# Optimization experiments

Measured on AMD Instinct MI355X. Metric: run time of the kernel, lower is better.

Reference implementation:

```python
import jax, jax.numpy as jnp
import numpy as np

N = 50000   # nodes
E = 800000  # edges
D = 64      # hidden_channels (= in_channels)
L = 3       # num_layers
G = 512     # graphs in batch
S = 32      # s_channels
BN_EPS = 1e-5


def setup_inputs() -> dict:
    key = jax.random.key(0)
    ks = jax.random.split(key, 10)
    x = jax.random.normal(ks[0], (N, D), dtype=jnp.float32)
    edge_index = jax.random.randint(ks[1], (2, E), 0, N)
    batch = jnp.sort(jax.random.randint(ks[2], (N,), 0, G))
    mapping = jax.random.randint(ks[3], (G,), 0, N)
    edge_weight = jax.random.uniform(ks[4], (E,), dtype=jnp.float32)
    pooling_mask = jnp.ones((N,), dtype=jnp.float32)
    # per-layer GIN MLP params (stacked over layers)
    W1 = 0.05 * jax.random.normal(ks[5], (L, D, D), dtype=jnp.float32)
    b1 = jnp.zeros((L, D), jnp.float32)
    gamma = jnp.ones((L, D), jnp.float32)
    beta = jnp.zeros((L, D), jnp.float32)
    bn_mean = jnp.zeros((L, D), jnp.float32)
    bn_var = jnp.ones((L, D), jnp.float32)
    W2 = 0.05 * jax.random.normal(ks[6], (L, D, D), dtype=jnp.float32)
    b2 = jnp.zeros((L, D), jnp.float32)
    eps = jnp.zeros((L,), jnp.float32)  # train_eps=True, init 0
    lin_w = 0.05 * jax.random.normal(ks[7], (2 * D * L, S), dtype=jnp.float32)
    lin_b = jnp.zeros((S,), jnp.float32)
    return dict(x=x, edge_weight=edge_weight, pooling_mask=pooling_mask,
                W1=W1, b1=b1, gamma=gamma, beta=beta, bn_mean=bn_mean,
                bn_var=bn_var, W2=W2, b2=b2, eps=eps, lin_w=lin_w,
                lin_b=lin_b, edge_index=edge_index, batch=batch,
                mapping=mapping)


def _sgin_forward(x, edge_weight, pooling_mask, W1, b1, gamma, beta,
                  bn_mean, bn_var, W2, b2, eps, lin_w, lin_b,
                  edge_index, batch, mapping):
    src, dst = edge_index[0], edge_index[1]
    h = x  # dropout is identity in eval mode
    pooled = []
    for i in range(L):
        # GIN aggregation: sum_j w_ij * h_j  at target nodes
        msg = h[src] * edge_weight[:, None]            # [E, D]
        agg = jax.ops.segment_sum(msg, dst, num_segments=N)
        z = (1.0 + eps[i]) * h + agg                   # [N, D]
        # MLP: Linear -> BN(eval) -> ReLU -> Linear -> ReLU
        z = z @ W1[i] + b1[i]
        z = gamma[i] * (z - bn_mean[i]) * jax.lax.rsqrt(bn_var[i] + BN_EPS) + beta[i]
        z = jax.nn.relu(z)
        h = jax.nn.relu(z @ W2[i] + b2[i])
        # per-layer pooling: masked global add pool || center-node gather
        emb_add = jax.ops.segment_sum(h * pooling_mask[:, None], batch,
                                      num_segments=G)  # [G, D]
        emb_center = h[mapping]                          # [G, D]
        pooled.append(jnp.concatenate([emb_add, emb_center], axis=-1))
    hcat = jnp.concatenate(pooled, axis=1)               # [G, 2*D*L]
    return hcat @ lin_w + lin_b                          # [G, S]


def reference(x, edge_weight, pooling_mask, W1, b1, gamma, beta, bn_mean,
              bn_var, W2, b2, eps, lin_w, lin_b, edge_index, batch, mapping):
    return _sgin_forward(x, edge_weight, pooling_mask, W1, b1, gamma, beta,
                         bn_mean, bn_var, W2, b2, eps, lin_w, lin_b,
                         edge_index, batch, mapping)
```

## Files before the change

kernel.cpp:

```cpp
#include <hip/hip_runtime.h>
#include <hip/hip_fp16.h>

#define DD 64
#define HC 384
#define SS 32
#define BINW 256
#define BSH 8
#define CAP 8192
#define CHUNK 2048

typedef _Float16 f16x8v __attribute__((ext_vector_type(8)));
typedef float f32x4v __attribute__((ext_vector_type(4)));

__global__ __launch_bounds__(256) void prep_kernel(
    const float* __restrict__ x, __half* __restrict__ hh0,
    int* __restrict__ bin_cur, float* __restrict__ hcat,
    const float* __restrict__ W1, const float* __restrict__ W2,
    const float* __restrict__ gma, const float* __restrict__ bta,
    const float* __restrict__ bnm, const float* __restrict__ bnv,
    const float* __restrict__ b1, __half* __restrict__ wpk,
    float* __restrict__ abbn, int nbins, int hcat4, int total)
{
  int gid = blockIdx.x * 256 + threadIdx.x;
  if (gid < nbins) bin_cur[gid] = gid * CAP;
  if (gid < hcat4) ((float4*)hcat)[gid] = make_float4(0.f, 0.f, 0.f, 0.f);
  if (gid < 3072) {
    int lane_ = gid & 63;
    int rest = gid >> 6;
    int kb = rest & 1;
    int nt = (rest >> 1) & 3;
    int gm = (rest >> 3) & 1;
    int ly = rest >> 4;
    const float* W = gm ? W2 : W1;
    int c = nt * 16 + (lane_ & 15);
    int k0 = kb * 32 + (lane_ >> 4) * 8;
    f16x8v o;
    #pragma unroll
    for (int j = 0; j < 8; ++j)
      o[j] = (_Float16)W[((size_t)ly * DD + k0 + j) * DD + c];
    *(f16x8v*)(wpk + gid * 8) = o;
  }
  if (gid >= 4096 && gid < 4288) {
    int id = gid - 4096;
    int ly = id >> 6, c = id & 63;
    float A = gma[ly * DD + c] * rsqrtf(bnv[ly * DD + c] + 1e-5f);
    float B = fmaf(b1[ly * DD + c] - bnm[ly * DD + c], A, bta[ly * DD + c]);
    abbn[ly * 128 + c] = A;
    abbn[ly * 128 + 64 + c] = B;
  }
  int i = gid * 8;
  if (i < total) {
    float4 a = *(const float4*)(x + i);
    float4 b = *(const float4*)(x + i + 4);
    __half2 o[4];
    o[0] = __floats2half2_rn(a.x, a.y);
    o[1] = __floats2half2_rn(a.z, a.w);
    o[2] = __floats2half2_rn(b.x, b.y);
    o[3] = __floats2half2_rn(b.z, b.w);
    *(float4*)(hh0 + i) = *(float4*)o;
  }
}

__global__ __launch_bounds__(256) void bin_part_kernel(
    const int* __restrict__ ei, const float* __restrict__ ew,
    int* __restrict__ bin_cur, unsigned* __restrict__ pk_slab,
    unsigned short* __restrict__ dl_slab, int E)
{
  __shared__ unsigned spk[CHUNK];
  __shared__ unsigned short sdst[CHUNK];
  __shared__ int bcnt[256], boff[256], bcur[256], gbase[256], stmp[256];
  int t = threadIdx.x;
  int e0 = blockIdx.x * CHUNK;
  int m = min(CHUNK, E - e0);
  bcnt[t] = 0;
  __syncthreads();
  for (int i = t; i < m; i += 256)
    atomicAdd(&bcnt[ei[E + e0 + i] >> BSH], 1);
  __syncthreads();
  int v = bcnt[t];
  stmp[t] = v;
  __syncthreads();
  for (int o = 1; o < 256; o <<= 1) {
    int u = (t >= o) ? stmp[t - o] : 0;
    __syncthreads();
    stmp[t] += u;
    __syncthreads();
  }
  boff[t] = stmp[t] - v;
  bcur[t] = stmp[t] - v;
  if (v > 0) gbase[t] = atomicAdd(&bin_cur[t], v);
  __syncthreads();
  for (int i = t; i < m; i += 256) {
    unsigned d = (unsigned)ei[E + e0 + i];
    int b = d >> BSH;
    int p = atomicAdd(&bcur[b], 1);
    unsigned short wh = __half_as_ushort(__float2half(ew[e0 + i]));
    spk[p] = (unsigned)ei[e0 + i] | ((unsigned)wh << 16);
    sdst[p] = (unsigned short)d;
  }
  __syncthreads();
  for (int i = t; i < m; i += 256) {
    unsigned short d = sdst[i];
    int b = d >> BSH;
    int g = gbase[b] + (i - boff[b]);
    pk_slab[g] = spk[i];
    dl_slab[g] = d;
  }
}

__global__ __launch_bounds__(256) void fine_csr_kernel(
    const unsigned* __restrict__ pk_slab,
    const unsigned short* __restrict__ dl_slab,
    const int* __restrict__ bin_cur, int* __restrict__ beg,
    int* __restrict__ endo, unsigned* __restrict__ packed, int N)
{
  __shared__ int cnt[256], loff[256], cur[256], stmp[256];
  int t = threadIdx.x;
  int b = blockIdx.x;
  int sbase = b * CAP;
  int m = bin_cur[b] - sbase;
  cnt[t] = 0;
  __syncthreads();
  for (int i = t; i < m; i += 256)
    atomicAdd(&cnt[dl_slab[sbase + i] & 255], 1);
  __syncthreads();
  int v = cnt[t];
  stmp[t] = v;
  __syncthreads();
  for (int o = 1; o < 256; o <<= 1) {
    int u = (t >= o) ? stmp[t - o] : 0;
    __syncthreads();
    stmp[t] += u;
    __syncthreads();
  }
  loff[t] = stmp[t] - v;
  cur[t] = loff[t];
  int node = b * BINW + t;
  if (node < N) {
    beg[node] = sbase + loff[t];
    endo[node] = sbase + loff[t] + v;
  }
  __syncthreads();
  for (int i = t; i < m; i += 256) {
    int dl = dl_slab[sbase + i] & 255;
    int p = atomicAdd(&cur[dl], 1);
    packed[sbase + p] = pk_slab[sbase + i];
  }
}

__global__ __launch_bounds__(256) void gather_kernel(
    const __half* __restrict__ hh, const unsigned* __restrict__ packed,
    const int* __restrict__ begA, const int* __restrict__ endA,
    const float* __restrict__ epsv, __half* __restrict__ zh, int layer, int N)
{
  int wave = threadIdx.x >> 6;
  int lane = threadIdx.x & 63;
  int sub = lane >> 3;
  int ch0 = (lane & 7) * 8;
  int na = blockIdx.x * 8 + wave * 2;
  int nb = na + 1;
  if (na >= N) return;
  bool hasB = nb < N;
  int bega = begA[na], enda = endA[na];
  int begb = hasB ? begA[nb] : 0, endb = hasB ? endA[nb] : 0;
  float accA[8] = {0, 0, 0, 0, 0, 0, 0, 0};
  float accB[8] = {0, 0, 0, 0, 0, 0, 0, 0};
  int ea = bega + sub, eb = begb + sub;
  while (ea < enda || eb < endb) {
    bool va = ea < enda;
    bool vb = eb < endb;
    unsigned pa = 0, pb = 0;
    if (va) pa = packed[ea];
    if (vb) pb = packed[eb];
    float4 ra, rb;
    if (va) ra = *(const float4*)(hh + (size_t)(pa & 0xffffu) * DD + ch0);
    if (vb) rb = *(const float4*)(hh + (size_t)(pb & 0xffffu) * DD + ch0);
    if (va) {
      float w = __half2float(__ushort_as_half((unsigned short)(pa >> 16)));
      const __half2* H = (const __half2*)&ra;
      #pragma unroll
      for (int j = 0; j < 4; ++j) {
        float2 f = __half22float2(H[j]);
        accA[2 * j]     = fmaf(w, f.x, accA[2 * j]);
        accA[2 * j + 1] = fmaf(w, f.y, accA[2 * j + 1]);
      }
    }
    if (vb) {
      float w = __half2float(__ushort_as_half((unsigned short)(pb >> 16)));
      const __half2* H = (const __half2*)&rb;
      #pragma unroll
      for (int j = 0; j < 4; ++j) {
        float2 f = __half22float2(H[j]);
        accB[2 * j]     = fmaf(w, f.x, accB[2 * j]);
        accB[2 * j + 1] = fmaf(w, f.y, accB[2 * j + 1]);
      }
    }
    ea += 8; eb += 8;
  }
  #pragma unroll
  for (int j = 0; j < 8; ++j) {
    accA[j] += __shfl_xor(accA[j], 8);
    accA[j] += __shfl_xor(accA[j], 16);
    accA[j] += __shfl_xor(accA[j], 32);
    accB[j] += __shfl_xor(accB[j], 8);
    accB[j] += __shfl_xor(accB[j], 16);
    accB[j] += __shfl_xor(accB[j], 32);
  }
  if (sub == 0) {
    float e1 = 1.0f + epsv[layer];
    {
      float4 sr = *(const float4*)(hh + (size_t)na * DD + ch0);
      const __half2* S = (const __half2*)&sr;
      f16x8v q;
      #pragma unroll
      for (int j = 0; j < 4; ++j) {
        float2 f = __half22float2(S[j]);
        q[2 * j]     = (_Float16)fmaf(e1, f.x, accA[2 * j]);
        q[2 * j + 1] = (_Float16)fmaf(e1, f.y, accA[2 * j + 1]);
      }
      *(f16x8v*)(zh + (size_t)na * DD + ch0) = q;
    }
    if (hasB) {
      float4 sr = *(const float4*)(hh + (size_t)nb * DD + ch0);
      const __half2* S = (const __half2*)&sr;
      f16x8v q;
      #pragma unroll
      for (int j = 0; j < 4; ++j) {
        float2 f = __half22float2(S[j]);
        q[2 * j]     = (_Float16)fmaf(e1, f.x, accB[2 * j]);
        q[2 * j + 1] = (_Float16)fmaf(e1, f.y, accB[2 * j + 1]);
      }
      *(f16x8v*)(zh + (size_t)nb * DD + ch0) = q;
    }
  }
}

__global__ __launch_bounds__(256) void node_mfma_kernel(
    const __half* __restrict__ zh, __half* __restrict__ hhout,
    const __half* __restrict__ wpk, const float* __restrict__ abbn,
    const float* __restrict__ b2, const float* __restrict__ pmask,
    const int* __restrict__ batch, float* __restrict__ hcat,
    int layer, int N)
{
  __shared__ float tileF[DD * DD];
  __half* tileH = (__half*)tileF;
  const int wave = threadIdx.x >> 6;
  const int lane = threadIdx.x & 63;
  const int g = lane >> 4;
  const int cr = lane & 15;
  const int n0 = blockIdx.x * 64;
  const int mrow = n0 + wave * 16 + cr;

  const __half* wl  = wpk + (size_t)layer * 8192;
  const __half* w2l = wl + 4096;

  f16x8v a0 = *(const f16x8v*)(zh + (size_t)mrow * DD + g * 8);
  f16x8v a1 = *(const f16x8v*)(zh + (size_t)mrow * DD + 32 + g * 8);
  f32x4v acc[4];
  #pragma unroll
  for (int nt = 0; nt < 4; ++nt) {
    f16x8v b0 = *(const f16x8v*)(wl + (nt * 2 + 0) * 512 + lane * 8);
    f16x8v b1 = *(const f16x8v*)(wl + (nt * 2 + 1) * 512 + lane * 8);
    acc[nt] = (f32x4v){0.f, 0.f, 0.f, 0.f};
    acc[nt] = __builtin_amdgcn_mfma_f32_16x16x32_f16(a0, b0, acc[nt], 0, 0, 0);
    acc[nt] = __builtin_amdgcn_mfma_f32_16x16x32_f16(a1, b1, acc[nt], 0, 0, 0);
  }
  #pragma unroll
  for (int nt = 0; nt < 4; ++nt) {
    int c = nt * 16 + cr;
    float Ab = abbn[layer * 128 + c];
    float Bb = abbn[layer * 128 + 64 + c];
    #pragma unroll
    for (int r = 0; r < 4; ++r) {
      int row = wave * 16 + g * 4 + r;
      float v = fmaxf(fmaf(acc[nt][r], Ab, Bb), 0.f);
      tileH[row * DD + (((c >> 3) ^ (row & 7)) * 8) + (c & 7)] = __float2half(v);
    }
  }
  __syncthreads();
  const int arow = wave * 16 + cr;
  f16x8v a20 = *(const f16x8v*)(tileH + arow * DD + ((g ^ (arow & 7)) * 8));
  f16x8v a21 = *(const f16x8v*)(tileH + arow * DD + (((4 + g) ^ (arow & 7)) * 8));
  f32x4v acc2[4];
  #pragma unroll
  for (int nt = 0; nt < 4; ++nt) {
    f16x8v b0 = *(const f16x8v*)(w2l + (nt * 2 + 0) * 512 + lane * 8);
    f16x8v b1 = *(const f16x8v*)(w2l + (nt * 2 + 1) * 512 + lane * 8);
    acc2[nt] = (f32x4v){0.f, 0.f, 0.f, 0.f};
    acc2[nt] = __builtin_amdgcn_mfma_f32_16x16x32_f16(a20, b0, acc2[nt], 0, 0, 0);
    acc2[nt] = __builtin_amdgcn_mfma_f32_16x16x32_f16(a21, b1, acc2[nt], 0, 0, 0);
  }
  __syncthreads();
  #pragma unroll
  for (int nt = 0; nt < 4; ++nt) {
    int c = nt * 16 + cr;
    float bb = b2[layer * DD + c];
    #pragma unroll
    for (int r = 0; r < 4; ++r) {
      int row = wave * 16 + g * 4 + r;
      tileF[row * DD + ((c + row) & 63)] = fmaxf(acc2[nt][r] + bb, 0.f);
    }
  }
  __syncthreads();
  #pragma unroll
  for (int i = 0; i < 2; ++i) {
    int id = i * 256 + threadIdx.x;
    int rw = id >> 3, q = id & 7;
    if (n0 + rw < N) {
      f16x8v hv;
      #pragma unroll
      for (int j = 0; j < 8; ++j)
        hv[j] = (_Float16)tileF[rw * DD + ((q * 8 + j + rw) & 63)];
      *(f16x8v*)(hhout + (size_t)(n0 + rw) * DD + q * 8) = hv;
    }
  }
  float accp = 0.0f;
  int gcur = -1;
  for (int i = 0; i < 16; ++i) {
    int r = wave * 16 + i;
    int n = n0 + r;
    if (n >= N) break;
    float v = tileF[r * DD + ((lane + r) & 63)];
    int gb = batch[n];
    if (gb != gcur) {
      if (gcur >= 0) atomicAdd(&hcat[gcur * HC + layer * 128 + lane], accp);
      gcur = gb; accp = 0.0f;
    }
    accp = fmaf(v, pmask[n], accp);
  }
  if (gcur >= 0) atomicAdd(&hcat[gcur * HC + layer * 128 + lane], accp);
}

__global__ __launch_bounds__(256) void final_kernel(
    const float* __restrict__ hcat, const __half* __restrict__ h1,
    const __half* __restrict__ h2, const __half* __restrict__ h3,
    const int* __restrict__ mapping, const float* __restrict__ lw,
    const float* __restrict__ lb, float* __restrict__ out, int G)
{
  int gid = blockIdx.x * 256 + threadIdx.x;
  int g = gid >> 5, s = gid & 31;
  if (g >= G) return;
  float acc = lb[s];
  size_t mrow = (size_t)mapping[g] * DD;
  #pragma unroll
  for (int l = 0; l < 3; ++l) {
    const float* hc = hcat + g * HC + l * 128;
    const float* lwa = lw + (l * 128) * SS + s;
    #pragma unroll 4
    for (int c = 0; c < 64; ++c)
      acc = fmaf(hc[c], lwa[c * SS], acc);
    const __half* hr = ((l == 0) ? h1 : ((l == 1) ? h2 : h3)) + mrow;
    const float* lwc = lw + (l * 128 + 64) * SS + s;
    #pragma unroll 4
    for (int c = 0; c < 64; ++c)
      acc = fmaf(__half2float(hr[c]), lwc[c * SS], acc);
  }
  out[g * SS + s] = acc;
}

extern "C" void kernel_launch(void* const* d_in, const int* in_sizes, int n_in,
                              void* d_out, int out_size, void* d_ws, size_t ws_size,
                              hipStream_t stream)
{
  const float* x     = (const float*)d_in[0];
  const float* ew    = (const float*)d_in[1];
  const float* pmask = (const float*)d_in[2];
  const float* W1    = (const float*)d_in[3];
  const float* b1    = (const float*)d_in[4];
  const float* gma   = (const float*)d_in[5];
  const float* bta   = (const float*)d_in[6];
  const float* bnm   = (const float*)d_in[7];
  const float* bnv   = (const float*)d_in[8];
  const float* W2    = (const float*)d_in[9];
  const float* b2    = (const float*)d_in[10];
  const float* epsv  = (const float*)d_in[11];
  const float* lw    = (const float*)d_in[12];
  const float* lb    = (const float*)d_in[13];
  const int*   ei    = (const int*)d_in[14];
  const int*   batch = (const int*)d_in[15];
  const int*   mapping = (const int*)d_in[16];

  const int N = in_sizes[2];
  const int E = in_sizes[1];
  const int G = in_sizes[16];
  const int nbins = (N + BINW - 1) / BINW;
  const int nchunks = (E + CHUNK - 1) / CHUNK;

  __half*   hh0  = (__half*)d_ws;
  __half*   hh1  = hh0 + (size_t)N * DD;
  __half*   hh2  = hh1 + (size_t)N * DD;
  __half*   hh3  = hh2 + (size_t)N * DD;
  float*    zslab = (float*)(hh3 + (size_t)N * DD);
  __half*   zh   = (__half*)zslab;
  float*    hcat = zslab + (size_t)N * DD;
  int*      beg  = (int*)(hcat + (size_t)G * HC);
  int*      endo = beg + N;
  int*      bin_cur = endo + N;
  unsigned* packed  = (unsigned*)(bin_cur + 256);
  unsigned* pk_slab = packed + (size_t)nbins * CAP;
  unsigned short* dl_slab =
      (unsigned short*)(pk_slab + (size_t)nbins * CAP);
  __half*   wpk  = (__half*)(dl_slab + (size_t)nbins * CAP);
  float*    abbn = (float*)(wpk + 24576);
  float* fout = (float*)d_out;

  prep_kernel<<<(N * DD / 8 + 255) / 256, 256, 0, stream>>>(
      x, hh0, bin_cur, hcat, W1, W2, gma, bta, bnm, bnv, b1,
      wpk, abbn, nbins, G * HC / 4, N * DD);

  bin_part_kernel<<<nchunks, 256, 0, stream>>>(ei, ew, bin_cur,
                                               pk_slab, dl_slab, E);
  fine_csr_kernel<<<nbins, 256, 0, stream>>>(pk_slab, dl_slab, bin_cur,
                                             beg, endo, packed, N);

  __half* hhs[4] = {hh0, hh1, hh2, hh3};
  for (int layer = 0; layer < 3; ++layer) {
    gather_kernel<<<(N + 7) / 8, 256, 0, stream>>>(
        hhs[layer], packed, beg, endo, epsv, zh, layer, N);
    node_mfma_kernel<<<(N + 63) / 64, 256, 0, stream>>>(
        zh, hhs[layer + 1], wpk, abbn, b2, pmask, batch, hcat, layer, N);
  }
  final_kernel<<<(G * SS + 255) / 256, 256, 0, stream>>>(
      hcat, hh1, hh2, hh3, mapping, lw, lb, fout, G);
}
```

Before: 256.7 us.

## Fuse edge gather aggregation into the per-layer MFMA MLP kernel

Merges the gather kernel and the node MLP kernel into one layer kernel. Each wave aggregates neighbours for 16 nodes, four at a time, and writes the combined z rows into a swizzled shared-memory tile instead of a global fp16 buffer. The MFMA layers then read from that tile. This removes the global round trip of z and one launch per layer, but each block now has only 64 nodes' worth of gather parallelism and more registers, which may lower occupancy and latency hiding for the random neighbour loads.

Result: slower. 319.9 us (+24.6%).

```diff
diff --git a/kernel.cpp b/kernel.cpp
--- a/kernel.cpp
+++ b/kernel.cpp
@@ -148,95 +148,10 @@
   }
 }
 
-__global__ __launch_bounds__(256) void gather_kernel(
+__global__ __launch_bounds__(256) void layer_kernel(
     const __half* __restrict__ hh, const unsigned* __restrict__ packed,
     const int* __restrict__ begA, const int* __restrict__ endA,
-    const float* __restrict__ epsv, __half* __restrict__ zh, int layer, int N)
-{
-  int wave = threadIdx.x >> 6;
-  int lane = threadIdx.x & 63;
-  int sub = lane >> 3;
-  int ch0 = (lane & 7) * 8;
-  int na = blockIdx.x * 8 + wave * 2;
-  int nb = na + 1;
-  if (na >= N) return;
-  bool hasB = nb < N;
-  int bega = begA[na], enda = endA[na];
-  int begb = hasB ? begA[nb] : 0, endb = hasB ? endA[nb] : 0;
-  float accA[8] = {0, 0, 0, 0, 0, 0, 0, 0};
-  float accB[8] = {0, 0, 0, 0, 0, 0, 0, 0};
-  int ea = bega + sub, eb = begb + sub;
-  while (ea < enda || eb < endb) {
-    bool va = ea < enda;
-    bool vb = eb < endb;
-    unsigned pa = 0, pb = 0;
-    if (va) pa = packed[ea];
-    if (vb) pb = packed[eb];
-    float4 ra, rb;
-    if (va) ra = *(const float4*)(hh + (size_t)(pa & 0xffffu) * DD + ch0);
-    if (vb) rb = *(const float4*)(hh + (size_t)(pb & 0xffffu) * DD + ch0);
-    if (va) {
-      float w = __half2float(__ushort_as_half((unsigned short)(pa >> 16)));
-      const __half2* H = (const __half2*)&ra;
-      #pragma unroll
-      for (int j = 0; j < 4; ++j) {
-        float2 f = __half22float2(H[j]);
-        accA[2 * j]     = fmaf(w, f.x, accA[2 * j]);
-        accA[2 * j + 1] = fmaf(w, f.y, accA[2 * j + 1]);
-      }
-    }
-    if (vb) {
-      float w = __half2float(__ushort_as_half((unsigned short)(pb >> 16)));
-      const __half2* H = (const __half2*)&rb;
-      #pragma unroll
-      for (int j = 0; j < 4; ++j) {
-        float2 f = __half22float2(H[j]);
-        accB[2 * j]     = fmaf(w, f.x, accB[2 * j]);
-        accB[2 * j + 1] = fmaf(w, f.y, accB[2 * j + 1]);
-      }
-    }
-    ea += 8; eb += 8;
-  }
-  #pragma unroll
-  for (int j = 0; j < 8; ++j) {
-    accA[j] += __shfl_xor(accA[j], 8);
-    accA[j] += __shfl_xor(accA[j], 16);
-    accA[j] += __shfl_xor(accA[j], 32);
-    accB[j] += __shfl_xor(accB[j], 8);
-    accB[j] += __shfl_xor(accB[j], 16);
-    accB[j] += __shfl_xor(accB[j], 32);
-  }
-  if (sub == 0) {
-    float e1 = 1.0f + epsv[layer];
-    {
-      float4 sr = *(const float4*)(hh + (size_t)na * DD + ch0);
-      const __half2* S = (const __half2*)&sr;
-      f16x8v q;
-      #pragma unroll
-      for (int j = 0; j < 4; ++j) {
-        float2 f = __half22float2(S[j]);
-        q[2 * j]     = (_Float16)fmaf(e1, f.x, accA[2 * j]);
-        q[2 * j + 1] = (_Float16)fmaf(e1, f.y, accA[2 * j + 1]);
-      }
-      *(f16x8v*)(zh + (size_t)na * DD + ch0) = q;
-    }
-    if (hasB) {
-      float4 sr = *(const float4*)(hh + (size_t)nb * DD + ch0);
-      const __half2* S = (const __half2*)&sr;
-      f16x8v q;
-      #pragma unroll
-      for (int j = 0; j < 4; ++j) {
-        float2 f = __half22float2(S[j]);
-        q[2 * j]     = (_Float16)fmaf(e1, f.x, accB[2 * j]);
-        q[2 * j + 1] = (_Float16)fmaf(e1, f.y, accB[2 * j + 1]);
-      }
-      *(f16x8v*)(zh + (size_t)nb * DD + ch0) = q;
-    }
-  }
-}
-
-__global__ __launch_bounds__(256) void node_mfma_kernel(
-    const __half* __restrict__ zh, __half* __restrict__ hhout,
+    const float* __restrict__ epsv, __half* __restrict__ hhout,
     const __half* __restrict__ wpk, const float* __restrict__ abbn,
     const float* __restrict__ b2, const float* __restrict__ pmask,
     const int* __restrict__ batch, float* __restrict__ hcat,
@@ -244,26 +159,95 @@
 {
   __shared__ float tileF[DD * DD];
   __half* tileH = (__half*)tileF;
+  __half* zT = ((__half*)tileF) + 4096;
   const int wave = threadIdx.x >> 6;
   const int lane = threadIdx.x & 63;
+  const int sub = lane >> 3;
+  const int q8 = lane & 7;
+  const int ch0 = q8 * 8;
+  const int n0 = blockIdx.x * 64;
+  const float e1 = 1.0f + epsv[layer];
+
+  for (int p = 0; p < 4; ++p) {
+    int nbase = n0 + wave * 16 + p * 4;
+    float acc[4][8];
+    int e[4], en[4];
+    #pragma unroll
+    for (int c = 0; c < 4; ++c) {
+      int n = nbase + c;
+      bool valid = n < N;
+      e[c] = valid ? begA[n] + sub : 0;
+      en[c] = valid ? endA[n] : 0;
+      #pragma unroll
+      for (int j = 0; j < 8; ++j) acc[c][j] = 0.f;
+    }
+    while (e[0] < en[0] || e[1] < en[1] || e[2] < en[2] || e[3] < en[3]) {
+      #pragma unroll
+      for (int c = 0; c < 4; ++c) {
+        if (e[c] < en[c]) {
+          unsigned pk = packed[e[c]];
+          float4 r = *(const float4*)(hh + (size_t)(pk & 0xffffu) * DD + ch0);
+          float w = __half2float(__ushort_as_half((unsigned short)(pk >> 16)));
+          const __half2* H = (const __half2*)&r;
+          #pragma unroll
+          for (int j = 0; j < 4; ++j) {
+            float2 f = __half22float2(H[j]);
+            acc[c][2 * j]     = fmaf(w, f.x, acc[c][2 * j]);
+            acc[c][2 * j + 1] = fmaf(w, f.y, acc[c][2 * j + 1]);
+          }
+        }
+        e[c] += 8;
+      }
+    }
+    #pragma unroll
+    for (int c = 0; c < 4; ++c)
+      #pragma unroll
+      for (int j = 0; j < 8; ++j) {
+        acc[c][j] += __shfl_xor(acc[c][j], 8);
+        acc[c][j] += __shfl_xor(acc[c][j], 16);
+        acc[c][j] += __shfl_xor(acc[c][j], 32);
+      }
+    if (sub == 0) {
+      #pragma unroll
+      for (int c = 0; c < 4; ++c) {
+        int n = nbase + c;
+        int row = n - n0;
+        f16x8v qv;
+        if (n < N) {
+          float4 sr = *(const float4*)(hh + (size_t)n * DD + ch0);
+          const __half2* S = (const __half2*)&sr;
+          #pragma unroll
+          for (int j = 0; j < 4; ++j) {
+            float2 f = __half22float2(S[j]);
+            qv[2 * j]     = (_Float16)fmaf(e1, f.x, acc[c][2 * j]);
+            qv[2 * j + 1] = (_Float16)fmaf(e1, f.y, acc[c][2 * j + 1]);
+          }
+        } else {
+          #pragma unroll
+          for (int j = 0; j < 8; ++j) qv[j] = (_Float16)0.f;
+        }
+        *(f16x8v*)(zT + row * DD + ((q8 ^ (row & 7)) * 8)) = qv;
+      }
+    }
+  }
+  __syncthreads();
+
   const int g = lane >> 4;
   const int cr = lane & 15;
-  const int n0 = blockIdx.x * 64;
-  const int mrow = n0 + wave * 16 + cr;
-
+  const int arow = wave * 16 + cr;
   const __half* wl  = wpk + (size_t)layer * 8192;
   const __half* w2l = wl + 4096;
 
-  f16x8v a0 = *(const f16x8v*)(zh + (size_t)mrow * DD + g * 8);
-  f16x8v a1 = *(const f16x8v*)(zh + (size_t)mrow * DD + 32 + g * 8);
-  f32x4v acc[4];
+  f16x8v a0 = *(const f16x8v*)(zT + arow * DD + ((g ^ (cr & 7)) * 8));
+  f16x8v a1 = *(const f16x8v*)(zT + arow * DD + (((g + 4) ^ (cr & 7)) * 8));
+  f32x4v acc1[4];
   #pragma unroll
   for (int nt = 0; nt < 4; ++nt) {
     f16x8v b0 = *(const f16x8v*)(wl + (nt * 2 + 0) * 512 + lane * 8);
     f16x8v b1 = *(const f16x8v*)(wl + (nt * 2 + 1) * 512 + lane * 8);
-    acc[nt] = (f32x4v){0.f, 0.f, 0.f, 0.f};
-    acc[nt] = __builtin_amdgcn_mfma_f32_16x16x32_f16(a0, b0, acc[nt], 0, 0, 0);
-    acc[nt] = __builtin_amdgcn_mfma_f32_16x16x32_f16(a1, b1, acc[nt], 0, 0, 0);
+    acc1[nt] = (f32x4v){0.f, 0.f, 0.f, 0.f};
+    acc1[nt] = __builtin_amdgcn_mfma_f32_16x16x32_f16(a0, b0, acc1[nt], 0, 0, 0);
+    acc1[nt] = __builtin_amdgcn_mfma_f32_16x16x32_f16(a1, b1, acc1[nt], 0, 0, 0);
   }
   #pragma unroll
   for (int nt = 0; nt < 4; ++nt) {
@@ -273,12 +257,11 @@
     #pragma unroll
     for (int r = 0; r < 4; ++r) {
       int row = wave * 16 + g * 4 + r;
-      float v = fmaxf(fmaf(acc[nt][r], Ab, Bb), 0.f);
+      float v = fmaxf(fmaf(acc1[nt][r], Ab, Bb), 0.f);
       tileH[row * DD + (((c >> 3) ^ (row & 7)) * 8) + (c & 7)] = __float2half(v);
     }
   }
   __syncthreads();
-  const int arow = wave * 16 + cr;
   f16x8v a20 = *(const f16x8v*)(tileH + arow * DD + ((g ^ (arow & 7)) * 8));
   f16x8v a21 = *(const f16x8v*)(tileH + arow * DD + (((4 + g) ^ (arow & 7)) * 8));
   f32x4v acc2[4];
@@ -390,9 +373,7 @@
   __half*   hh1  = hh0 + (size_t)N * DD;
   __half*   hh2  = hh1 + (size_t)N * DD;
   __half*   hh3  = hh2 + (size_t)N * DD;
-  float*    zslab = (float*)(hh3 + (size_t)N * DD);
-  __half*   zh   = (__half*)zslab;
-  float*    hcat = zslab + (size_t)N * DD;
+  float*    hcat = (float*)(hh3 + (size_t)N * DD);
   int*      beg  = (int*)(hcat + (size_t)G * HC);
   int*      endo = beg + N;
   int*      bin_cur = endo + N;
@@ -415,10 +396,9 @@
 
   __half* hhs[4] = {hh0, hh1, hh2, hh3};
   for (int layer = 0; layer < 3; ++layer) {
-    gather_kernel<<<(N + 7) / 8, 256, 0, stream>>>(
-        hhs[layer], packed, beg, endo, epsv, zh, layer, N);
-    node_mfma_kernel<<<(N + 63) / 64, 256, 0, stream>>>(
-        zh, hhs[layer + 1], wpk, abbn, b2, pmask, batch, hcat, layer, N);
+    layer_kernel<<<(N + 63) / 64, 256, 0, stream>>>(
+        hhs[layer], packed, beg, endo, epsv, hhs[layer + 1],
+        wpk, abbn, b2, pmask, batch, hcat, layer, N);
   }
   final_kernel<<<(G * SS + 255) / 256, 256, 0, stream>>>(
       hcat, hh1, hh2, hh3, mapping, lw, lb, fout, G);
```
